# Kernel optimization log

Measured on AMD Instinct MI355X. Metric: run time of the kernel, lower is better.

The kernel has to match this reference:

```python
import jax, jax.numpy as jnp
import numpy as np

H = 12          # num_attention_heads
D = 768         # hidden_size
R = 4           # channel_shrink_ratio
DH = D // H     # 64, attention_head_size
DL = D // R     # 192, layout hidden size
DHL = DH // R   # 16, layout head size
NEG = jnp.finfo(jnp.float32).min


def setup_inputs() -> dict:
    key = jax.random.key(0)
    ks = jax.random.split(key, 16)
    B, S = 8, 1024
    s = 0.02
    inp = {
        "hidden_states": jax.random.normal(ks[0], (B, S, D), jnp.float32),
        "layout_hidden_states": jax.random.normal(ks[1], (B, S, DL), jnp.float32),
        "attention_mask": jnp.ones((B, S), jnp.float32),
        "Wq": jax.random.normal(ks[2], (D, D), jnp.float32) * s,
        "bq": jnp.zeros((D,), jnp.float32),
        "Wk": jax.random.normal(ks[3], (D, D), jnp.float32) * s,
        "bk": jnp.zeros((D,), jnp.float32),
        "Wv": jax.random.normal(ks[4], (D, D), jnp.float32) * s,
        "bv": jnp.zeros((D,), jnp.float32),
        "Wlq": jax.random.normal(ks[5], (DL, DL), jnp.float32) * s,
        "blq": jnp.zeros((DL,), jnp.float32),
        "Wlk": jax.random.normal(ks[6], (DL, DL), jnp.float32) * s,
        "blk": jnp.zeros((DL,), jnp.float32),
        "Wlv": jax.random.normal(ks[7], (DL, DL), jnp.float32) * s,
        "blv": jnp.zeros((DL,), jnp.float32),
    }
    return inp


def _heads(x, hd):
    # [B,S,H*hd] -> [B,H,S,hd]
    B, S, _ = x.shape
    return x.reshape(B, S, H, hd).transpose(0, 2, 1, 3)


def reference(hidden_states, layout_hidden_states, attention_mask,
              Wq, bq, Wk, bk, Wv, bv, Wlq, blq, Wlk, blk, Wlv, blv):
    B, S, _ = hidden_states.shape
    q = _heads(hidden_states @ Wq.T + bq, DH)
    k = _heads(hidden_states @ Wk.T + bk, DH)
    v = _heads(hidden_states @ Wv.T + bv, DH)
    lq = _heads(layout_hidden_states @ Wlq.T + blq, DHL)
    lk = _heads(layout_hidden_states @ Wlk.T + blk, DHL)
    lv = _heads(layout_hidden_states @ Wlv.T + blv, DHL)

    scores = jnp.einsum('bhqd,bhkd->bhqk', q, k) / jnp.sqrt(jnp.float32(DH))
    lscores = jnp.einsum('bhqd,bhkd->bhqk', lq, lk) / jnp.sqrt(jnp.float32(DHL))
    fused = scores + lscores  # cross-added scores (same for both streams)

    bias = (1.0 - attention_mask)[:, None, None, :] * NEG  # [B,1,1,S]
    fused = fused + bias

    probs = jax.nn.softmax(fused, axis=-1)   # dropout disabled (p=0)

    ctx = jnp.einsum('bhqk,bhkd->bhqd', probs, v)
    ctx = ctx.transpose(0, 2, 1, 3).reshape(B, S, D)
    lctx = jnp.einsum('bhqk,bhkd->bhqd', probs, lv)
    lctx = lctx.transpose(0, 2, 1, 3).reshape(B, S, DL)
    return ctx, lctx, probs
```

## Files before the change

kernel.cpp:

```cpp
#include <hip/hip_runtime.h>

#define NH   12
#define SEQ  1024
#define NB   8
#define DCAT 96
#define DV   80

typedef __attribute__((ext_vector_type(8))) short  bf16x8;
typedef __attribute__((ext_vector_type(4))) float  f32x4;
typedef __attribute__((ext_vector_type(4))) unsigned short u16x4;

static __device__ __forceinline__ unsigned short f2bf(float x) {
    unsigned int u = __float_as_uint(x);
    u += 0x7fffu + ((u >> 16) & 1u);
    return (unsigned short)(u >> 16);
}
static __device__ __forceinline__ f32x4 fzero() {
    f32x4 z; z[0]=0.f; z[1]=0.f; z[2]=0.f; z[3]=0.f; return z;
}
static __device__ __forceinline__ unsigned int cvtpk(float lo, float hi) {
    unsigned int r;
    asm("v_cvt_pk_bf16_f32 %0, %1, %2" : "=v"(r) : "v"(lo), "v"(hi));
    return r;
}

#define GLDS16(gp, lp) __builtin_amdgcn_global_load_lds(                      \
    (const __attribute__((address_space(1))) void*)(gp),                      \
    (__attribute__((address_space(3))) void*)(lp), 16, 0, 0)

#define WAITV(nstr) asm volatile("s_waitcnt vmcnt(" nstr ")" ::: "memory")
#define SBARRIER() do {                                                       \
    __builtin_amdgcn_sched_barrier(0);                                        \
    asm volatile("" ::: "memory");                                            \
    __builtin_amdgcn_s_barrier();                                             \
    asm volatile("" ::: "memory");                                            \
    __builtin_amdgcn_sched_barrier(0);                                        \
} while (0)

__global__ __launch_bounds__(256) void cvt_all(
    const float* __restrict__ hs, const float* __restrict__ lhs,
    const float* __restrict__ Wq, const float* __restrict__ Wk, const float* __restrict__ Wv,
    const float* __restrict__ Wlq, const float* __restrict__ Wlk, const float* __restrict__ Wlv,
    unsigned short* __restrict__ hid16, unsigned short* __restrict__ lay16,
    unsigned short* __restrict__ wqkv16, unsigned short* __restrict__ wl16)
{
    int i = blockIdx.x * 256 + threadIdx.x;
    const float* src; unsigned short* dst; int off;
    if      (i < 1572864) { src = hs;  dst = hid16;           off = i; }
    else if (i < 1966080) { src = lhs; dst = lay16;           off = i - 1572864; }
    else if (i < 2113536) { src = Wq;  dst = wqkv16;          off = i - 1966080; }
    else if (i < 2260992) { src = Wk;  dst = wqkv16 + 589824; off = i - 2113536; }
    else if (i < 2408448) { src = Wv;  dst = wqkv16 + 1179648;off = i - 2260992; }
    else if (i < 2417664) { src = Wlq; dst = wl16;            off = i - 2408448; }
    else if (i < 2426880) { src = Wlk; dst = wl16 + 36864;    off = i - 2417664; }
    else if (i < 2436096) { src = Wlv; dst = wl16 + 73728;    off = i - 2426880; }
    else return;
    f32x4 v = ((const f32x4*)src)[off];
    u16x4 o;
    o[0] = f2bf(v[0]); o[1] = f2bf(v[1]); o[2] = f2bf(v[2]); o[3] = f2bf(v[3]);
    ((u16x4*)dst)[off] = o;
}

__global__ __launch_bounds__(256) void proj_gemm(
    const unsigned short* __restrict__ Ahid,
    const unsigned short* __restrict__ Alay,
    const unsigned short* __restrict__ Bwqkv,
    const unsigned short* __restrict__ Bwl,
    const float* __restrict__ bq, const float* __restrict__ bk, const float* __restrict__ bv,
    const float* __restrict__ blq, const float* __restrict__ blk_, const float* __restrict__ blv,
    unsigned short* __restrict__ Qc, unsigned short* __restrict__ Kc, unsigned short* __restrict__ VT)
{
    __shared__ __align__(16) unsigned short As[4096];
    __shared__ __align__(16) unsigned short Bs[4096];
    const int tid = threadIdx.x, w = tid >> 6, lane = tid & 63;
    const int g = lane >> 4, c = lane & 15;

    const int variant = (blockIdx.y < 18) ? 0 : 1;
    const unsigned short* A  = variant ? Alay : Ahid;
    const unsigned short* Bw = variant ? Bwl  : Bwqkv;
    const float* b0 = variant ? blq  : bq;
    const float* b1 = variant ? blk_ : bk;
    const float* b2 = variant ? blv  : bv;
    const int K    = variant ? 192 : 768;
    const int Ntot = variant ? 576 : 2304;
    const int m0 = blockIdx.x * 128;
    const int n0 = (variant ? (blockIdx.y - 18) : blockIdx.y) * 128;

    const int wr = w >> 1, wc = w & 1;
    const int srow = lane >> 2, scol = (lane & 3) * 8;

    f32x4 acc[4][4];
    #pragma unroll
    for (int m = 0; m < 4; m++)
        #pragma unroll
        for (int n = 0; n < 4; n++) acc[m][n] = fzero();

    const int ch0 = w * 2, ch1 = w * 2 + 1;
    const size_t arow0 = (size_t)(m0 + ch0 * 16 + srow) * K + scol;
    const size_t arow1 = (size_t)(m0 + ch1 * 16 + srow) * K + scol;
    int bn0 = n0 + ch0 * 16 + srow; if (bn0 >= Ntot) bn0 = Ntot - 1;
    int bn1 = n0 + ch1 * 16 + srow; if (bn1 >= Ntot) bn1 = Ntot - 1;
    const size_t brow0 = (size_t)bn0 * K + scol;
    const size_t brow1 = (size_t)bn1 * K + scol;

    for (int k0 = 0; k0 < K; k0 += 32) {
        __syncthreads();
        GLDS16(A  + arow0 + k0, As + ch0 * 512);
        GLDS16(A  + arow1 + k0, As + ch1 * 512);
        GLDS16(Bw + brow0 + k0, Bs + ch0 * 512);
        GLDS16(Bw + brow1 + k0, Bs + ch1 * 512);
        __syncthreads();
        bf16x8 af[4], bfr[4];
        #pragma unroll
        for (int m = 0; m < 4; m++) af[m]  = *(const bf16x8*)&As[(wr*64 + m*16 + c)*32 + g*8];
        #pragma unroll
        for (int n = 0; n < 4; n++) bfr[n] = *(const bf16x8*)&Bs[(wc*64 + n*16 + c)*32 + g*8];
        #pragma unroll
        for (int m = 0; m < 4; m++)
            #pragma unroll
            for (int n = 0; n < 4; n++)
                acc[m][n] = __builtin_amdgcn_mfma_f32_16x16x32_bf16(af[m], bfr[n], acc[m][n], 0, 0, 0);
    }

    const int b_ = m0 >> 10;
    #pragma unroll
    for (int nf = 0; nf < 4; nf++) {
        int n = n0 + wc * 64 + nf * 16 + c;
        if (n >= Ntot) continue;
        int seg, nn;
        if (variant == 0) { seg = (n >= 1536) ? 2 : ((n >= 768) ? 1 : 0); nn = n - seg * 768; }
        else              { seg = (n >= 384)  ? 2 : ((n >= 192) ? 1 : 0); nn = n - seg * 192; }
        const float* bp = (seg == 0) ? b0 : ((seg == 1) ? b1 : b2);
        float bv = bp[nn];
        float scale = (seg == 0) ? (variant ? 0.25f : 0.125f) : 1.0f;
        int h, d;
        if (variant == 0) { h = nn >> 6; d = nn & 63; }
        else              { h = nn >> 4; d = 64 + (nn & 15); }
        #pragma unroll
        for (int m = 0; m < 4; m++) {
            int row = m0 + wr * 64 + m * 16 + 4 * g;
            int s = row & 1023;
            if (seg < 2) {
                unsigned short* dst = (seg == 0) ? Qc : Kc;
                size_t base = (size_t)(b_ * NH + h) * SEQ;
                #pragma unroll
                for (int r = 0; r < 4; r++) {
                    dst[(base + s + r) * DCAT + d] = f2bf((acc[m][nf][r] + bv) * scale);
                    if (variant == 1)
                        dst[(base + s + r) * DCAT + d + 16] = 0;
                }
            } else {
                u16x4 pk;
                #pragma unroll
                for (int r = 0; r < 4; r++) pk[r] = f2bf(acc[m][nf][r] + bv);
                int kb = s >> 5, ko = s & 31;
                *(u16x4*)&VT[(((size_t)(b_ * NH + h) * 32 + kb) * DV + d) * 32 + ko] = pk;
            }
        }
    }
}

__global__ __launch_bounds__(256, 3) void attn_kernel(
    const unsigned short* __restrict__ Qc,
    const unsigned short* __restrict__ Kc,
    const unsigned short* __restrict__ VT,
    const float* __restrict__ mask,
    float* __restrict__ ctx,
    float* __restrict__ lctx,
    float* __restrict__ probs)
{
    __shared__ __align__(16) unsigned short Ks[2 * 6144];
    __shared__ __align__(16) unsigned short pbuf[4][32][36];

    const int tid = threadIdx.x, w = tid >> 6, lane = tid & 63;
    const int g = lane >> 4, c = lane & 15;

    const int bid = blockIdx.x;
    const int xc = bid & 7, j = bid >> 3;
    const int bh = xc + 8 * (j >> 3);
    const int qt = j & 7;
    const int b = bh / NH, h = bh % NH;
    const int qrb = qt * 128 + w * 32;
    const float NEGF = -3.4028234663852886e38f;

    bf16x8 qa0, qa1, qa2, qb0, qb1, qb2;
    {
        const unsigned short* qr0 = &Qc[((size_t)bh * SEQ + qrb + c) * DCAT + g * 8];
        qa0 = *(const bf16x8*)(qr0);
        qa1 = *(const bf16x8*)(qr0 + 32);
        qa2 = *(const bf16x8*)(qr0 + 64);
        const unsigned short* qr1 = qr0 + 16 * DCAT;
        qb0 = *(const bf16x8*)(qr1);
        qb1 = *(const bf16x8*)(qr1 + 32);
        qb2 = *(const bf16x8*)(qr1 + 64);
    }
    const unsigned short* Kb = Kc + (size_t)bh * SEQ * DCAT;
    const unsigned short* Vb = VT + (size_t)bh * 32 * DV * 32;
    const float* mk = mask + b * SEQ;

    const int slot8 = (g ^ ((c >> 1) & 3)) * 8;

    const unsigned short* gsrc[3]; int gstep[3];
    #pragma unroll
    for (int r = 0; r < 3; r++) {
        const int m = tid + 256 * r;
        if (m < 384) {
            int p = m >> 7, row = (m >> 2) & 31, jj = m & 3;
            int jx = jj ^ ((row >> 1) & 3);
            gsrc[r]  = Kb + row * DCAT + p * 32 + jx * 8;
            gstep[r] = 32 * DCAT;
        } else if (m < 704) {
            int mv = m - 384;
            int df = mv >> 6, cc = (mv >> 2) & 15, jj = mv & 3;
            int jx = jj ^ ((cc >> 1) & 3);
            gsrc[r]  = Vb + (df * 16 + cc) * 32 + jx * 8;
            gstep[r] = DV * 32;
        } else {
            gsrc[r]  = Vb;
            gstep[r] = 0;
        }
    }
    const int dub = w * 512;

    f32x4 cacc0[5], cacc1[5];
    #pragma unroll
    for (int nf = 0; nf < 5; nf++) { cacc0[nf] = fzero(); cacc1[nf] = fzero(); }
    float sm0 = 0.f, sm1 = 0.f;

    #pragma unroll
    for (int r = 0; r < 3; r++)
        GLDS16(gsrc[r], Ks + r * 2048 + dub);
    __builtin_amdgcn_sched_barrier(0);

    for (int t = 0; t < 32; t++) {
        const int buf = t & 1;
        if (t == 0) WAITV("0");
        else        WAITV("2");
        SBARRIER();
        if (t < 31) {
            #pragma unroll
            for (int r = 0; r < 3; r++)
                GLDS16(gsrc[r] + (t + 1) * gstep[r], Ks + (buf ^ 1) * 6144 + r * 2048 + dub);
            __builtin_amdgcn_sched_barrier(0);
        }

        #pragma unroll
        for (int ktl = 0; ktl < 2; ktl++) {
            const int rb = buf * 6144 + (ktl * 16 + c) * 32 + slot8;
            bf16x8 k0 = *(const bf16x8*)&Ks[rb];
            bf16x8 k1 = *(const bf16x8*)&Ks[rb + 1024];
            bf16x8 k2 = *(const bf16x8*)&Ks[rb + 2048];
            f32x4 m4 = *(const f32x4*)&mk[t * 32 + ktl * 16 + 4 * g];
            __builtin_amdgcn_s_setprio(1);
            f32x4 a0 = __builtin_amdgcn_mfma_f32_16x16x32_bf16(k0, qa0, fzero(), 0, 0, 0);
            f32x4 a1 = __builtin_amdgcn_mfma_f32_16x16x32_bf16(k1, qa1, fzero(), 0, 0, 0);
            f32x4 a2 = __builtin_amdgcn_mfma_f32_16x16x32_bf16(k2, qa2, fzero(), 0, 0, 0);
            f32x4 b0 = __builtin_amdgcn_mfma_f32_16x16x32_bf16(k0, qb0, fzero(), 0, 0, 0);
            f32x4 b1 = __builtin_amdgcn_mfma_f32_16x16x32_bf16(k1, qb1, fzero(), 0, 0, 0);
            f32x4 b2 = __builtin_amdgcn_mfma_f32_16x16x32_bf16(k2, qb2, fzero(), 0, 0, 0);
            __builtin_amdgcn_s_setprio(0);
            f32x4 e0, e1;
            #pragma unroll
            for (int r = 0; r < 4; r++) {
                float bias = (1.0f - m4[r]) * NEGF;
                e0[r] = __expf(a0[r] + a1[r] + a2[r] + bias);
                e1[r] = __expf(b0[r] + b1[r] + b2[r] + bias);
                sm0 += e0[r];
                sm1 += e1[r];
            }
            uint2 hh0, hh1;
            hh0.x = cvtpk(e0[0], e0[1]); hh0.y = cvtpk(e0[2], e0[3]);
            hh1.x = cvtpk(e1[0], e1[1]); hh1.y = cvtpk(e1[2], e1[3]);
            *(uint2*)&pbuf[w][c][ktl * 16 + 4 * g]      = hh0;
            *(uint2*)&pbuf[w][16 + c][ktl * 16 + 4 * g] = hh1;
        }
        const int vb0 = buf * 6144 + 3072 + c * 32 + slot8;
        bf16x8 vf0 = *(const bf16x8*)&Ks[vb0];
        bf16x8 vf1 = *(const bf16x8*)&Ks[vb0 + 512];
        bf16x8 vf2 = *(const bf16x8*)&Ks[vb0 + 1024];
        bf16x8 vf3 = *(const bf16x8*)&Ks[vb0 + 1536];
        bf16x8 vf4 = *(const bf16x8*)&Ks[vb0 + 2048];
        bf16x8 pa0 = *(const bf16x8*)&pbuf[w][c][g * 8];
        bf16x8 pa1 = *(const bf16x8*)&pbuf[w][16 + c][g * 8];
        __builtin_amdgcn_s_setprio(1);
        cacc0[0] = __builtin_amdgcn_mfma_f32_16x16x32_bf16(pa0, vf0, cacc0[0], 0, 0, 0);
        cacc1[0] = __builtin_amdgcn_mfma_f32_16x16x32_bf16(pa1, vf0, cacc1[0], 0, 0, 0);
        cacc0[1] = __builtin_amdgcn_mfma_f32_16x16x32_bf16(pa0, vf1, cacc0[1], 0, 0, 0);
        cacc1[1] = __builtin_amdgcn_mfma_f32_16x16x32_bf16(pa1, vf1, cacc1[1], 0, 0, 0);
        cacc0[2] = __builtin_amdgcn_mfma_f32_16x16x32_bf16(pa0, vf2, cacc0[2], 0, 0, 0);
        cacc1[2] = __builtin_amdgcn_mfma_f32_16x16x32_bf16(pa1, vf2, cacc1[2], 0, 0, 0);
        cacc0[3] = __builtin_amdgcn_mfma_f32_16x16x32_bf16(pa0, vf3, cacc0[3], 0, 0, 0);
        cacc1[3] = __builtin_amdgcn_mfma_f32_16x16x32_bf16(pa1, vf3, cacc1[3], 0, 0, 0);
        cacc0[4] = __builtin_amdgcn_mfma_f32_16x16x32_bf16(pa0, vf4, cacc0[4], 0, 0, 0);
        cacc1[4] = __builtin_amdgcn_mfma_f32_16x16x32_bf16(pa1, vf4, cacc1[4], 0, 0, 0);
        __builtin_amdgcn_s_setprio(0);
    }

    sm0 += __shfl_xor(sm0, 16); sm0 += __shfl_xor(sm0, 32);
    sm1 += __shfl_xor(sm1, 16); sm1 += __shfl_xor(sm1, 32);
    const float rinv0 = 1.0f / fmaxf(sm0, 1e-38f);
    const float rinv1 = 1.0f / fmaxf(sm1, 1e-38f);

    float rl0[4], rl1[4];
    #pragma unroll
    for (int r = 0; r < 4; r++) {
        rl0[r] = __shfl(rinv0, 4 * g + r);
        rl1[r] = __shfl(rinv1, 4 * g + r);
    }

    #pragma unroll
    for (int nf = 0; nf < 4; nf++)
        #pragma unroll
        for (int r = 0; r < 4; r++) {
            int q0 = qrb + 4 * g + r;
            ctx[((size_t)(b * SEQ + q0)) * 768 + h * 64 + nf * 16 + c] = cacc0[nf][r] * rl0[r];
            ctx[((size_t)(b * SEQ + q0 + 16)) * 768 + h * 64 + nf * 16 + c] = cacc1[nf][r] * rl1[r];
        }
    #pragma unroll
    for (int r = 0; r < 4; r++) {
        int q0 = qrb + 4 * g + r;
        lctx[((size_t)(b * SEQ + q0)) * 192 + h * 16 + c] = cacc0[4][r] * rl0[r];
        lctx[((size_t)(b * SEQ + q0 + 16)) * 192 + h * 16 + c] = cacc1[4][r] * rl1[r];
    }

    const int srow   = lane >> 2;
    const int schunk = (lane & 3) ^ ((lane >> 3) & 3);
    const int ssrcA  = (w * 16 + srow) * DCAT + schunk * 8;
    unsigned short* sdstA = &Ks[w * 512];

    const size_t prow0 = ((size_t)bh * SEQ + qrb + c) * SEQ;
    const size_t prow1 = prow0 + 16 * SEQ;

    SBARRIER();
    #pragma unroll
    for (int p = 0; p < 3; p++) GLDS16(Kb + ssrcA + p * 32, sdstA + p * 2048);
    __builtin_amdgcn_sched_barrier(0);

    for (int t = 0; t < 16; t++) {
        const int buf = t & 1;
        if (t == 0) WAITV("0");
        else        WAITV("12");
        SBARRIER();
        if (t < 15) {
            const unsigned short* src = Kb + (t + 1) * 6144 + ssrcA;
            unsigned short* dst = sdstA + (buf ^ 1) * 6144;
            #pragma unroll
            for (int p = 0; p < 3; p++) GLDS16(src + p * 32, dst + p * 2048);
            __builtin_amdgcn_sched_barrier(0);
        }
        #pragma unroll
        for (int ktl = 0; ktl < 4; ktl++) {
            const int rb = buf * 6144 + (ktl * 16 + c) * 32 + slot8;
            bf16x8 k0 = *(const bf16x8*)&Ks[rb];
            bf16x8 k1 = *(const bf16x8*)&Ks[rb + 2048];
            bf16x8 k2 = *(const bf16x8*)&Ks[rb + 4096];
            f32x4 m4 = *(const f32x4*)&mk[t * 64 + ktl * 16 + 4 * g];
            __builtin_amdgcn_s_setprio(1);
            f32x4 a0 = __builtin_amdgcn_mfma_f32_16x16x32_bf16(k0, qa0, fzero(), 0, 0, 0);
            f32x4 a1 = __builtin_amdgcn_mfma_f32_16x16x32_bf16(k1, qa1, fzero(), 0, 0, 0);
            f32x4 a2 = __builtin_amdgcn_mfma_f32_16x16x32_bf16(k2, qa2, fzero(), 0, 0, 0);
            f32x4 b0 = __builtin_amdgcn_mfma_f32_16x16x32_bf16(k0, qb0, fzero(), 0, 0, 0);
            f32x4 b1 = __builtin_amdgcn_mfma_f32_16x16x32_bf16(k1, qb1, fzero(), 0, 0, 0);
            f32x4 b2 = __builtin_amdgcn_mfma_f32_16x16x32_bf16(k2, qb2, fzero(), 0, 0, 0);
            __builtin_amdgcn_s_setprio(0);
            f32x4 p0, p1;
            #pragma unroll
            for (int r = 0; r < 4; r++) {
                float bias = (1.0f - m4[r]) * NEGF;
                p0[r] = __expf(a0[r] + a1[r] + a2[r] + bias) * rinv0;
                p1[r] = __expf(b0[r] + b1[r] + b2[r] + bias) * rinv1;
            }
            *(f32x4*)&probs[prow0 + (t * 64 + ktl * 16) + 4 * g] = p0;
            *(f32x4*)&probs[prow1 + (t * 64 + ktl * 16) + 4 * g] = p1;
        }
    }
}

extern "C" void kernel_launch(void* const* d_in, const int* in_sizes, int n_in,
                              void* d_out, int out_size, void* d_ws, size_t ws_size,
                              hipStream_t stream)
{
    const float* hs   = (const float*)d_in[0];
    const float* lhs  = (const float*)d_in[1];
    const float* mask = (const float*)d_in[2];
    const float* Wq   = (const float*)d_in[3];
    const float* bq   = (const float*)d_in[4];
    const float* Wk   = (const float*)d_in[5];
    const float* bk   = (const float*)d_in[6];
    const float* Wv   = (const float*)d_in[7];
    const float* bv   = (const float*)d_in[8];
    const float* Wlq  = (const float*)d_in[9];
    const float* blq  = (const float*)d_in[10];
    const float* Wlk  = (const float*)d_in[11];
    const float* blk_ = (const float*)d_in[12];
    const float* Wlv  = (const float*)d_in[13];
    const float* blv  = (const float*)d_in[14];

    float* out   = (float*)d_out;
    float* ctx   = out;
    float* lctx  = out + (size_t)NB * SEQ * 768;
    float* probs = out + (size_t)NB * SEQ * 768 + (size_t)NB * SEQ * 192;

    char* ws = (char*)d_ws;
    unsigned short* Qc     = (unsigned short*)(ws);
    unsigned short* Kc     = (unsigned short*)(ws + 18874368);
    unsigned short* VT     = (unsigned short*)(ws + 37748736);
    unsigned short* hid16  = (unsigned short*)(ws + 53477376);
    unsigned short* lay16  = (unsigned short*)(ws + 66060288);
    unsigned short* wqkv16 = (unsigned short*)(ws + 69206016);
    unsigned short* wl16   = (unsigned short*)(ws + 72744960);

    cvt_all<<<dim3(9516), dim3(256), 0, stream>>>(hs, lhs, Wq, Wk, Wv, Wlq, Wlk, Wlv,
                                                  hid16, lay16, wqkv16, wl16);

    proj_gemm<<<dim3(64, 23), dim3(256), 0, stream>>>(hid16, lay16, wqkv16, wl16,
                                                      bq, bk, bv, blq, blk_, blv,
                                                      Qc, Kc, VT);

    attn_kernel<<<dim3(768), dim3(256), 0, stream>>>(Qc, Kc, VT, mask, ctx, lctx, probs);
}
```

Measured before the change: 237.3 us.

## Fold attention mask bias into padded Q/K column and drop setprio

Adds a small kernel that writes the mask bias into a spare padding column of K and a constant 1.0 into the matching Q column, so the QK^T MFMA produces the biased score directly. The attention kernels no longer load the mask or add the bias per element. The change also removes the s_setprio hints and alters the vmcnt wait counts. The price is one extra launch, plus the bias being rounded to bf16. The dropped bias add assumes column 80 previously held zeros and was otherwise unused, and rounding -FLT_MAX to bf16 may overflow to -inf.

```diff
diff --git a/kernel.cpp b/kernel.cpp
--- a/kernel.cpp
+++ b/kernel.cpp
@@ -61,6 +61,20 @@
     ((u16x4*)dst)[off] = o;
 }
 
+__global__ __launch_bounds__(256) void pad_fill(
+    const float* __restrict__ mask,
+    unsigned short* __restrict__ Qc, unsigned short* __restrict__ Kc)
+{
+    int i = blockIdx.x * 256 + threadIdx.x;
+    if (i >= 98304) return;
+    int bh = i >> 10, s = i & 1023;
+    int b = bh / NH;
+    float bias = (1.0f - mask[b * SEQ + s]) * -3.4028234663852886e38f;
+    size_t idx = ((size_t)bh * SEQ + s) * DCAT + 80;
+    Kc[idx] = f2bf(bias);
+    Qc[idx] = 0x3F80;
+}
+
 __global__ __launch_bounds__(256) void proj_gemm(
     const unsigned short* __restrict__ Ahid,
     const unsigned short* __restrict__ Alay,
@@ -164,7 +178,6 @@
     const unsigned short* __restrict__ Qc,
     const unsigned short* __restrict__ Kc,
     const unsigned short* __restrict__ VT,
-    const float* __restrict__ mask,
     float* __restrict__ ctx,
     float* __restrict__ lctx,
     float* __restrict__ probs)
@@ -181,7 +194,6 @@
     const int qt = j & 7;
     const int b = bh / NH, h = bh % NH;
     const int qrb = qt * 128 + w * 32;
-    const float NEGF = -3.4028234663852886e38f;
 
     bf16x8 qa0, qa1, qa2, qb0, qb1, qb2;
     {
@@ -196,7 +208,6 @@
     }
     const unsigned short* Kb = Kc + (size_t)bh * SEQ * DCAT;
     const unsigned short* Vb = VT + (size_t)bh * 32 * DV * 32;
-    const float* mk = mask + b * SEQ;
 
     const int slot8 = (g ^ ((c >> 1) & 3)) * 8;
 
@@ -234,8 +245,7 @@
 
     for (int t = 0; t < 32; t++) {
         const int buf = t & 1;
-        if (t == 0) WAITV("0");
-        else        WAITV("2");
+        WAITV("0");
         SBARRIER();
         if (t < 31) {
             #pragma unroll
@@ -250,21 +260,17 @@
             bf16x8 k0 = *(const bf16x8*)&Ks[rb];
             bf16x8 k1 = *(const bf16x8*)&Ks[rb + 1024];
             bf16x8 k2 = *(const bf16x8*)&Ks[rb + 2048];
-            f32x4 m4 = *(const f32x4*)&mk[t * 32 + ktl * 16 + 4 * g];
-            __builtin_amdgcn_s_setprio(1);
             f32x4 a0 = __builtin_amdgcn_mfma_f32_16x16x32_bf16(k0, qa0, fzero(), 0, 0, 0);
             f32x4 a1 = __builtin_amdgcn_mfma_f32_16x16x32_bf16(k1, qa1, fzero(), 0, 0, 0);
             f32x4 a2 = __builtin_amdgcn_mfma_f32_16x16x32_bf16(k2, qa2, fzero(), 0, 0, 0);
             f32x4 b0 = __builtin_amdgcn_mfma_f32_16x16x32_bf16(k0, qb0, fzero(), 0, 0, 0);
             f32x4 b1 = __builtin_amdgcn_mfma_f32_16x16x32_bf16(k1, qb1, fzero(), 0, 0, 0);
             f32x4 b2 = __builtin_amdgcn_mfma_f32_16x16x32_bf16(k2, qb2, fzero(), 0, 0, 0);
-            __builtin_amdgcn_s_setprio(0);
             f32x4 e0, e1;
             #pragma unroll
             for (int r = 0; r < 4; r++) {
-                float bias = (1.0f - m4[r]) * NEGF;
-                e0[r] = __expf(a0[r] + a1[r] + a2[r] + bias);
-                e1[r] = __expf(b0[r] + b1[r] + b2[r] + bias);
+                e0[r] = __expf(a0[r] + a1[r] + a2[r]);
+                e1[r] = __expf(b0[r] + b1[r] + b2[r]);
                 sm0 += e0[r];
                 sm1 += e1[r];
             }
@@ -282,7 +288,6 @@
         bf16x8 vf4 = *(const bf16x8*)&Ks[vb0 + 2048];
         bf16x8 pa0 = *(const bf16x8*)&pbuf[w][c][g * 8];
         bf16x8 pa1 = *(const bf16x8*)&pbuf[w][16 + c][g * 8];
-        __builtin_amdgcn_s_setprio(1);
         cacc0[0] = __builtin_amdgcn_mfma_f32_16x16x32_bf16(pa0, vf0, cacc0[0], 0, 0, 0);
         cacc1[0] = __builtin_amdgcn_mfma_f32_16x16x32_bf16(pa1, vf0, cacc1[0], 0, 0, 0);
         cacc0[1] = __builtin_amdgcn_mfma_f32_16x16x32_bf16(pa0, vf1, cacc0[1], 0, 0, 0);
@@ -293,7 +298,6 @@
         cacc1[3] = __builtin_amdgcn_mfma_f32_16x16x32_bf16(pa1, vf3, cacc1[3], 0, 0, 0);
         cacc0[4] = __builtin_amdgcn_mfma_f32_16x16x32_bf16(pa0, vf4, cacc0[4], 0, 0, 0);
         cacc1[4] = __builtin_amdgcn_mfma_f32_16x16x32_bf16(pa1, vf4, cacc1[4], 0, 0, 0);
-        __builtin_amdgcn_s_setprio(0);
     }
 
     sm0 += __shfl_xor(sm0, 16); sm0 += __shfl_xor(sm0, 32);
@@ -339,7 +343,7 @@
     for (int t = 0; t < 16; t++) {
         const int buf = t & 1;
         if (t == 0) WAITV("0");
-        else        WAITV("12");
+        else        WAITV("8");
         SBARRIER();
         if (t < 15) {
             const unsigned short* src = Kb + (t + 1) * 6144 + ssrcA;
@@ -354,21 +358,17 @@
             bf16x8 k0 = *(const bf16x8*)&Ks[rb];
             bf16x8 k1 = *(const bf16x8*)&Ks[rb + 2048];
             bf16x8 k2 = *(const bf16x8*)&Ks[rb + 4096];
-            f32x4 m4 = *(const f32x4*)&mk[t * 64 + ktl * 16 + 4 * g];
-            __builtin_amdgcn_s_setprio(1);
             f32x4 a0 = __builtin_amdgcn_mfma_f32_16x16x32_bf16(k0, qa0, fzero(), 0, 0, 0);
             f32x4 a1 = __builtin_amdgcn_mfma_f32_16x16x32_bf16(k1, qa1, fzero(), 0, 0, 0);
             f32x4 a2 = __builtin_amdgcn_mfma_f32_16x16x32_bf16(k2, qa2, fzero(), 0, 0, 0);
             f32x4 b0 = __builtin_amdgcn_mfma_f32_16x16x32_bf16(k0, qb0, fzero(), 0, 0, 0);
             f32x4 b1 = __builtin_amdgcn_mfma_f32_16x16x32_bf16(k1, qb1, fzero(), 0, 0, 0);
             f32x4 b2 = __builtin_amdgcn_mfma_f32_16x16x32_bf16(k2, qb2, fzero(), 0, 0, 0);
-            __builtin_amdgcn_s_setprio(0);
             f32x4 p0, p1;
             #pragma unroll
             for (int r = 0; r < 4; r++) {
-                float bias = (1.0f - m4[r]) * NEGF;
-                p0[r] = __expf(a0[r] + a1[r] + a2[r] + bias) * rinv0;
-                p1[r] = __expf(b0[r] + b1[r] + b2[r] + bias) * rinv1;
+                p0[r] = __expf(a0[r] + a1[r] + a2[r]) * rinv0;
+                p1[r] = __expf(b0[r] + b1[r] + b2[r]) * rinv1;
             }
             *(f32x4*)&probs[prow0 + (t * 64 + ktl * 16) + 4 * g] = p0;
             *(f32x4*)&probs[prow1 + (t * 64 + ktl * 16) + 4 * g] = p1;
@@ -417,5 +417,7 @@
                                                       bq, bk, bv, blq, blk_, blv,
                                                       Qc, Kc, VT);
 
-    attn_kernel<<<dim3(768), dim3(256), 0, stream>>>(Qc, Kc, VT, mask, ctx, lctx, probs);
-}
+    pad_fill<<<dim3(384), dim3(256), 0, stream>>>(mask, Qc, Kc);
+
+    attn_kernel<<<dim3(768), dim3(256), 0, stream>>>(Qc, Kc, VT, ctx, lctx, probs);
+}
```

New measurement: 237.9 us. About the same (+0.3%).
